# Performance work log

Measured on AMD Instinct MI355X. Metric: run time of the kernel, lower is better.

The kernel has to match this reference:

```python
import jax, jax.numpy as jnp
import numpy as np
from functools import partial

MIN_LIKELIHOOD = 1e-09


@partial(jax.custom_vjp, nondiff_argnums=(1,))
def lower_bound_toward(x, bound):
    return jnp.maximum(x, bound)

def _lbt_fwd(x, bound):
    return jnp.maximum(x, bound), x

def _lbt_bwd(bound, x, g):
    # gradient passes if input above bound, or gradient pushes x toward the bound
    pass_through = (x >= bound) | (g < 0)
    return (jnp.where(pass_through, g, jnp.zeros_like(g)),)

lower_bound_toward.defvjp(_lbt_fwd, _lbt_bwd)


def cdf_logits(x, Hs, As, Bs):
    # x: (C, 1, M). Per-channel tiny matmul chain with softplus/tanh gating.
    logits = x
    for H, a, b in zip(Hs, As, Bs):
        logits = jnp.einsum('cij,cjm->cim', jax.nn.softplus(H), logits) + b
        logits = logits + jnp.tanh(a) * jnp.tanh(logits)
    return logits


def setup_inputs() -> dict:
    key = jax.random.key(0)
    N, C, Hsp, W = 16, 320, 32, 32
    filters = (3, 3, 3)
    init_scale = 10.0
    fs = (1,) + filters + (1,)
    scale = init_scale ** (1.0 / (len(filters) + 1))
    keys = jax.random.split(key, len(filters) + 2)
    inp = {'x': jax.random.normal(keys[0], (N, C, Hsp, W), dtype=jnp.float32) * 3.0}
    for k in range(len(filters) + 1):
        H_init = float(np.log(np.expm1(1.0 / scale / fs[k + 1])))
        inp['H%d' % k] = jnp.full((C, fs[k + 1], fs[k]), H_init, dtype=jnp.float32)
        inp['a%d' % k] = jnp.zeros((C, fs[k + 1], 1), dtype=jnp.float32)
        inp['b%d' % k] = jax.random.uniform(keys[k + 1], (C, fs[k + 1], 1), dtype=jnp.float32, minval=-0.5, maxval=0.5)
    return inp


def reference(x, H0, H1, H2, H3, a0, a1, a2, a3, b0, b1, b2, b3):
    N, C, Hsp, W = x.shape
    Hs = (H0, H1, H2, H3)
    As = (a0, a1, a2, a3)
    Bs = (b0, b1, b2, b3)
    # (N,C,H,W) -> (C,1,N*H*W)
    lat = jnp.transpose(x, (1, 0, 2, 3)).reshape(C, 1, -1)
    cdf_upper = cdf_logits(lat + 0.5, Hs, As, Bs)
    cdf_lower = cdf_logits(lat - 0.5, Hs, As, Bs)
    sign = jax.lax.stop_gradient(-jnp.sign(cdf_upper + cdf_lower))
    like = jnp.abs(jax.nn.sigmoid(sign * cdf_upper) - jax.nn.sigmoid(sign * cdf_lower))
    like = jnp.transpose(like.reshape(C, N, Hsp, W), (1, 0, 2, 3))
    return lower_bound_toward(like, MIN_LIKELIHOOD)
```

## Files before the change

### kernel.cpp

```cpp
#include <hip/hip_runtime.h>
#include <math.h>


constexpr int HW = 1024;
constexpr float MINL = 1e-9f;

__device__ __forceinline__ float softplus_f(float v) {
    return fmaxf(v, 0.0f) + log1pf(expf(-fabsf(v)));
}

template<bool GATED>
__device__ __forceinline__ float cdf_t(float u, const float* q) {
    float y0 = fmaf(q[0], u, q[34]);
    float y1 = fmaf(q[1], u, q[35]);
    float y2 = fmaf(q[2], u, q[36]);
    if (GATED) {
        y0 = fmaf(q[24], tanhf(y0), y0);
        y1 = fmaf(q[25], tanhf(y1), y1);
        y2 = fmaf(q[26], tanhf(y2), y2);
    }
    float z0 = fmaf(q[3], y0, fmaf(q[4],  y1, fmaf(q[5],  y2, q[37])));
    float z1 = fmaf(q[6], y0, fmaf(q[7],  y1, fmaf(q[8],  y2, q[38])));
    float z2 = fmaf(q[9], y0, fmaf(q[10], y1, fmaf(q[11], y2, q[39])));
    if (GATED) {
        z0 = fmaf(q[27], tanhf(z0), z0);
        z1 = fmaf(q[28], tanhf(z1), z1);
        z2 = fmaf(q[29], tanhf(z2), z2);
    }
    float w0 = fmaf(q[12], z0, fmaf(q[13], z1, fmaf(q[14], z2, q[40])));
    float w1 = fmaf(q[15], z0, fmaf(q[16], z1, fmaf(q[17], z2, q[41])));
    float w2 = fmaf(q[18], z0, fmaf(q[19], z1, fmaf(q[20], z2, q[42])));
    if (GATED) {
        w0 = fmaf(q[30], tanhf(w0), w0);
        w1 = fmaf(q[31], tanhf(w1), w1);
        w2 = fmaf(q[32], tanhf(w2), w2);
    }
    float s = fmaf(q[21], w0, fmaf(q[22], w1, fmaf(q[23], w2, q[43])));
    if (GATED) s = fmaf(q[33], tanhf(s), s);
    return tanhf(0.5f * s);
}

template<bool GATED>
__device__ __forceinline__ float elem_like(float v, const float* q) {
    float tu = cdf_t<GATED>(v + 0.5f, q);
    float tl = cdf_t<GATED>(v - 0.5f, q);
    return fmaxf(0.5f * fabsf(tu - tl), MINL);
}

__global__ __launch_bounds__(256)
void hyperprior_density_kernel(
    const float* __restrict__ x,
    const float* __restrict__ H0, const float* __restrict__ a0, const float* __restrict__ b0,
    const float* __restrict__ H1, const float* __restrict__ a1, const float* __restrict__ b1,
    const float* __restrict__ H2, const float* __restrict__ a2, const float* __restrict__ b2,
    const float* __restrict__ H3, const float* __restrict__ a3, const float* __restrict__ b3,
    float* __restrict__ out, int C)
{
    __shared__ float p[44];
    const int c   = blockIdx.x;
    const int n   = blockIdx.y;
    const int tid = threadIdx.x;

    if (tid < 24) {
        float h;
        if      (tid < 3)  h = H0[c * 3 + tid];
        else if (tid < 12) h = H1[c * 9 + (tid - 3)];
        else if (tid < 21) h = H2[c * 9 + (tid - 12)];
        else               h = H3[c * 3 + (tid - 21)];
        p[tid] = softplus_f(h);
    } else if (tid < 34) {
        int i = tid - 24;
        float av;
        if      (i < 3) av = a0[c * 3 + i];
        else if (i < 6) av = a1[c * 3 + (i - 3)];
        else if (i < 9) av = a2[c * 3 + (i - 6)];
        else            av = a3[c];
        p[tid] = tanhf(av);
    } else if (tid < 44) {
        int i = tid - 34;
        float bv;
        if      (i < 3) bv = b0[c * 3 + i];
        else if (i < 6) bv = b1[c * 3 + (i - 3)];
        else if (i < 9) bv = b2[c * 3 + (i - 6)];
        else            bv = b3[c];
        p[tid] = bv;
    }
    __syncthreads();

    float q[44];
#pragma unroll
    for (int i = 0; i < 44; ++i) q[i] = p[i];

    bool gated = false;
#pragma unroll
    for (int i = 24; i < 34; ++i) gated = gated || (q[i] != 0.0f);

    const size_t base = ((size_t)n * (size_t)C + (size_t)c) * (size_t)HW;
    const float4* xin = reinterpret_cast<const float4*>(x + base);
    float4*       op  = reinterpret_cast<float4*>(out + base);

    float4 v = xin[tid];
    float4 r;
    if (!gated) {
        r.x = elem_like<false>(v.x, q);
        r.y = elem_like<false>(v.y, q);
        r.z = elem_like<false>(v.z, q);
        r.w = elem_like<false>(v.w, q);
    } else {
        r.x = elem_like<true>(v.x, q);
        r.y = elem_like<true>(v.y, q);
        r.z = elem_like<true>(v.z, q);
        r.w = elem_like<true>(v.w, q);
    }
    op[tid] = r;
}

extern "C" void kernel_launch(void* const* d_in, const int* in_sizes, int n_in,
                              void* d_out, int out_size, void* d_ws, size_t ws_size,
                              hipStream_t stream) {
    const float* x  = (const float*)d_in[0];
    const float* H0 = (const float*)d_in[1];
    const float* a0 = (const float*)d_in[2];
    const float* b0 = (const float*)d_in[3];
    const float* H1 = (const float*)d_in[4];
    const float* a1 = (const float*)d_in[5];
    const float* b1 = (const float*)d_in[6];
    const float* H2 = (const float*)d_in[7];
    const float* a2 = (const float*)d_in[8];
    const float* b2 = (const float*)d_in[9];
    const float* H3 = (const float*)d_in[10];
    const float* a3 = (const float*)d_in[11];
    const float* b3 = (const float*)d_in[12];
    float* out = (float*)d_out;

    const int C = in_sizes[1] / 3;
    const int N = in_sizes[0] / (C * HW);

    dim3 grid(C, N);
    hipLaunchKernelGGL(hyperprior_density_kernel, grid, dim3(256), 0, stream,
                       x, H0, a0, b0, H1, a1, b1, H2, a2, b2, H3, a3, b3, out, C);
}
```

Baseline: 102.7 us.

## Precompute per-channel parameters in a prep kernel and use fast tanh

New measurement: 103.4 us. Within noise of the previous version (+0.6%).

```diff
diff --git a/kernel.cpp b/kernel.cpp
--- a/kernel.cpp
+++ b/kernel.cpp
@@ -2,117 +2,133 @@
 #include <math.h>
 
 
-constexpr int HW = 1024;
+constexpr int HW   = 1024;
+constexpr int NPAR = 44;
+constexpr int PSTR = 48;
 constexpr float MINL = 1e-9f;
 
 __device__ __forceinline__ float softplus_f(float v) {
     return fmaxf(v, 0.0f) + log1pf(expf(-fabsf(v)));
 }
 
-template<bool GATED>
-__device__ __forceinline__ float cdf_t(float u, const float* q) {
-    float y0 = fmaf(q[0], u, q[34]);
-    float y1 = fmaf(q[1], u, q[35]);
-    float y2 = fmaf(q[2], u, q[36]);
-    if (GATED) {
-        y0 = fmaf(q[24], tanhf(y0), y0);
-        y1 = fmaf(q[25], tanhf(y1), y1);
-        y2 = fmaf(q[26], tanhf(y2), y2);
-    }
-    float z0 = fmaf(q[3], y0, fmaf(q[4],  y1, fmaf(q[5],  y2, q[37])));
-    float z1 = fmaf(q[6], y0, fmaf(q[7],  y1, fmaf(q[8],  y2, q[38])));
-    float z2 = fmaf(q[9], y0, fmaf(q[10], y1, fmaf(q[11], y2, q[39])));
-    if (GATED) {
-        z0 = fmaf(q[27], tanhf(z0), z0);
-        z1 = fmaf(q[28], tanhf(z1), z1);
-        z2 = fmaf(q[29], tanhf(z2), z2);
-    }
-    float w0 = fmaf(q[12], z0, fmaf(q[13], z1, fmaf(q[14], z2, q[40])));
-    float w1 = fmaf(q[15], z0, fmaf(q[16], z1, fmaf(q[17], z2, q[41])));
-    float w2 = fmaf(q[18], z0, fmaf(q[19], z1, fmaf(q[20], z2, q[42])));
-    if (GATED) {
-        w0 = fmaf(q[30], tanhf(w0), w0);
-        w1 = fmaf(q[31], tanhf(w1), w1);
-        w2 = fmaf(q[32], tanhf(w2), w2);
-    }
-    float s = fmaf(q[21], w0, fmaf(q[22], w1, fmaf(q[23], w2, q[43])));
-    if (GATED) s = fmaf(q[33], tanhf(s), s);
-    return tanhf(0.5f * s);
-}
-
-template<bool GATED>
-__device__ __forceinline__ float elem_like(float v, const float* q) {
-    float tu = cdf_t<GATED>(v + 0.5f, q);
-    float tl = cdf_t<GATED>(v - 0.5f, q);
-    return fmaxf(0.5f * fabsf(tu - tl), MINL);
+__device__ __forceinline__ float fast_tanh(float u) {
+    float e = __expf(-2.0f * fabsf(u));
+    float t = __fdividef(1.0f - e, 1.0f + e);
+    return copysignf(t, u);
 }
 
 __global__ __launch_bounds__(256)
-void hyperprior_density_kernel(
-    const float* __restrict__ x,
-    const float* __restrict__ H0, const float* __restrict__ a0, const float* __restrict__ b0,
-    const float* __restrict__ H1, const float* __restrict__ a1, const float* __restrict__ b1,
-    const float* __restrict__ H2, const float* __restrict__ a2, const float* __restrict__ b2,
-    const float* __restrict__ H3, const float* __restrict__ a3, const float* __restrict__ b3,
-    float* __restrict__ out, int C)
+void hp_prep(const float* __restrict__ H0, const float* __restrict__ a0, const float* __restrict__ b0,
+             const float* __restrict__ H1, const float* __restrict__ a1, const float* __restrict__ b1,
+             const float* __restrict__ H2, const float* __restrict__ a2, const float* __restrict__ b2,
+             const float* __restrict__ H3, const float* __restrict__ a3, const float* __restrict__ b3,
+             float* __restrict__ P, int C)
 {
-    __shared__ float p[44];
+    int t = blockIdx.x * 256 + threadIdx.x;
+    if (t >= C * NPAR) return;
+    int c = t / NPAR;
+    int i = t - c * NPAR;
+    float v;
+    if (i < 24) {
+        float h;
+        if      (i < 3)  h = H0[c * 3 + i];
+        else if (i < 12) h = H1[c * 9 + (i - 3)];
+        else if (i < 21) h = H2[c * 9 + (i - 12)];
+        else             h = H3[c * 3 + (i - 21)];
+        v = softplus_f(h);
+    } else if (i < 34) {
+        int j = i - 24; float a;
+        if      (j < 3) a = a0[c * 3 + j];
+        else if (j < 6) a = a1[c * 3 + (j - 3)];
+        else if (j < 9) a = a2[c * 3 + (j - 6)];
+        else            a = a3[c];
+        v = tanhf(a);
+    } else {
+        int j = i - 34; float b;
+        if      (j < 3) b = b0[c * 3 + j];
+        else if (j < 6) b = b1[c * 3 + (j - 3)];
+        else if (j < 9) b = b2[c * 3 + (j - 6)];
+        else            b = b3[c];
+        v = b;
+    }
+    P[c * PSTR + i] = v;
+}
+
+__global__ __launch_bounds__(256)
+void hp_main(const float* __restrict__ x, const float* __restrict__ P,
+             float* __restrict__ out, int C)
+{
     const int c   = blockIdx.x;
     const int n   = blockIdx.y;
     const int tid = threadIdx.x;
 
-    if (tid < 24) {
-        float h;
-        if      (tid < 3)  h = H0[c * 3 + tid];
-        else if (tid < 12) h = H1[c * 9 + (tid - 3)];
-        else if (tid < 21) h = H2[c * 9 + (tid - 12)];
-        else               h = H3[c * 3 + (tid - 21)];
-        p[tid] = softplus_f(h);
-    } else if (tid < 34) {
-        int i = tid - 24;
-        float av;
-        if      (i < 3) av = a0[c * 3 + i];
-        else if (i < 6) av = a1[c * 3 + (i - 3)];
-        else if (i < 9) av = a2[c * 3 + (i - 6)];
-        else            av = a3[c];
-        p[tid] = tanhf(av);
-    } else if (tid < 44) {
-        int i = tid - 34;
-        float bv;
-        if      (i < 3) bv = b0[c * 3 + i];
-        else if (i < 6) bv = b1[c * 3 + (i - 3)];
-        else if (i < 9) bv = b2[c * 3 + (i - 6)];
-        else            bv = b3[c];
-        p[tid] = bv;
-    }
-    __syncthreads();
+    const float* __restrict__ q = P + (size_t)c * PSTR;
+    const float k0 = q[0],  k1 = q[1],  k2 = q[2],  k3 = q[3],  k4 = q[4];
+    const float k5 = q[5],  k6 = q[6],  k7 = q[7],  k8 = q[8],  k9 = q[9];
+    const float k10 = q[10], k11 = q[11], k12 = q[12], k13 = q[13], k14 = q[14];
+    const float k15 = q[15], k16 = q[16], k17 = q[17], k18 = q[18], k19 = q[19];
+    const float k20 = q[20], k21 = q[21], k22 = q[22], k23 = q[23];
+    const float g0 = q[24], g1 = q[25], g2 = q[26], g3 = q[27], g4 = q[28];
+    const float g5 = q[29], g6 = q[30], g7 = q[31], g8 = q[32], g9 = q[33];
+    const float c0 = q[34], c1 = q[35], c2 = q[36], c3 = q[37], c4 = q[38];
+    const float c5 = q[39], c6 = q[40], c7 = q[41], c8 = q[42], c9 = q[43];
 
-    float q[44];
-#pragma unroll
-    for (int i = 0; i < 44; ++i) q[i] = p[i];
+    const bool gated = (g0 != 0.f) | (g1 != 0.f) | (g2 != 0.f) | (g3 != 0.f) |
+                       (g4 != 0.f) | (g5 != 0.f) | (g6 != 0.f) | (g7 != 0.f) |
+                       (g8 != 0.f) | (g9 != 0.f);
 
-    bool gated = false;
-#pragma unroll
-    for (int i = 24; i < 34; ++i) gated = gated || (q[i] != 0.0f);
+    auto cdfU = [&](float u) -> float {
+        float y0 = fmaf(k0, u, c0);
+        float y1 = fmaf(k1, u, c1);
+        float y2 = fmaf(k2, u, c2);
+        float z0 = fmaf(k3, y0, fmaf(k4,  y1, fmaf(k5,  y2, c3)));
+        float z1 = fmaf(k6, y0, fmaf(k7,  y1, fmaf(k8,  y2, c4)));
+        float z2 = fmaf(k9, y0, fmaf(k10, y1, fmaf(k11, y2, c5)));
+        float w0 = fmaf(k12, z0, fmaf(k13, z1, fmaf(k14, z2, c6)));
+        float w1 = fmaf(k15, z0, fmaf(k16, z1, fmaf(k17, z2, c7)));
+        float w2 = fmaf(k18, z0, fmaf(k19, z1, fmaf(k20, z2, c8)));
+        float s  = fmaf(k21, w0, fmaf(k22, w1, fmaf(k23, w2, c9)));
+        return fast_tanh(0.5f * s);
+    };
+    auto cdfG = [&](float u) -> float {
+        float y0 = fmaf(k0, u, c0);
+        float y1 = fmaf(k1, u, c1);
+        float y2 = fmaf(k2, u, c2);
+        y0 = fmaf(g0, fast_tanh(y0), y0);
+        y1 = fmaf(g1, fast_tanh(y1), y1);
+        y2 = fmaf(g2, fast_tanh(y2), y2);
+        float z0 = fmaf(k3, y0, fmaf(k4,  y1, fmaf(k5,  y2, c3)));
+        float z1 = fmaf(k6, y0, fmaf(k7,  y1, fmaf(k8,  y2, c4)));
+        float z2 = fmaf(k9, y0, fmaf(k10, y1, fmaf(k11, y2, c5)));
+        z0 = fmaf(g3, fast_tanh(z0), z0);
+        z1 = fmaf(g4, fast_tanh(z1), z1);
+        z2 = fmaf(g5, fast_tanh(z2), z2);
+        float w0 = fmaf(k12, z0, fmaf(k13, z1, fmaf(k14, z2, c6)));
+        float w1 = fmaf(k15, z0, fmaf(k16, z1, fmaf(k17, z2, c7)));
+        float w2 = fmaf(k18, z0, fmaf(k19, z1, fmaf(k20, z2, c8)));
+        w0 = fmaf(g6, fast_tanh(w0), w0);
+        w1 = fmaf(g7, fast_tanh(w1), w1);
+        w2 = fmaf(g8, fast_tanh(w2), w2);
+        float s = fmaf(k21, w0, fmaf(k22, w1, fmaf(k23, w2, c9)));
+        s = fmaf(g9, fast_tanh(s), s);
+        return fast_tanh(0.5f * s);
+    };
 
     const size_t base = ((size_t)n * (size_t)C + (size_t)c) * (size_t)HW;
-    const float4* xin = reinterpret_cast<const float4*>(x + base);
-    float4*       op  = reinterpret_cast<float4*>(out + base);
-
-    float4 v = xin[tid];
+    const float4 v = reinterpret_cast<const float4*>(x + base)[tid];
     float4 r;
     if (!gated) {
-        r.x = elem_like<false>(v.x, q);
-        r.y = elem_like<false>(v.y, q);
-        r.z = elem_like<false>(v.z, q);
-        r.w = elem_like<false>(v.w, q);
+        r.x = fmaxf(0.5f * fabsf(cdfU(v.x + 0.5f) - cdfU(v.x - 0.5f)), MINL);
+        r.y = fmaxf(0.5f * fabsf(cdfU(v.y + 0.5f) - cdfU(v.y - 0.5f)), MINL);
+        r.z = fmaxf(0.5f * fabsf(cdfU(v.z + 0.5f) - cdfU(v.z - 0.5f)), MINL);
+        r.w = fmaxf(0.5f * fabsf(cdfU(v.w + 0.5f) - cdfU(v.w - 0.5f)), MINL);
     } else {
-        r.x = elem_like<true>(v.x, q);
-        r.y = elem_like<true>(v.y, q);
-        r.z = elem_like<true>(v.z, q);
-        r.w = elem_like<true>(v.w, q);
+        r.x = fmaxf(0.5f * fabsf(cdfG(v.x + 0.5f) - cdfG(v.x - 0.5f)), MINL);
+        r.y = fmaxf(0.5f * fabsf(cdfG(v.y + 0.5f) - cdfG(v.y - 0.5f)), MINL);
+        r.z = fmaxf(0.5f * fabsf(cdfG(v.z + 0.5f) - cdfG(v.z - 0.5f)), MINL);
+        r.w = fmaxf(0.5f * fabsf(cdfG(v.w + 0.5f) - cdfG(v.w - 0.5f)), MINL);
     }
-    op[tid] = r;
+    reinterpret_cast<float4*>(out + base)[tid] = r;
 }
 
 extern "C" void kernel_launch(void* const* d_in, const int* in_sizes, int n_in,
@@ -132,11 +148,14 @@
     const float* a3 = (const float*)d_in[11];
     const float* b3 = (const float*)d_in[12];
     float* out = (float*)d_out;
+    float* P   = (float*)d_ws;
 
     const int C = in_sizes[1] / 3;
     const int N = in_sizes[0] / (C * HW);
 
-    dim3 grid(C, N);
-    hipLaunchKernelGGL(hyperprior_density_kernel, grid, dim3(256), 0, stream,
-                       x, H0, a0, b0, H1, a1, b1, H2, a2, b2, H3, a3, b3, out, C);
+    const int prep_items = C * NPAR;
+    hipLaunchKernelGGL(hp_prep, dim3((prep_items + 255) / 256), dim3(256), 0, stream,
+                       H0, a0, b0, H1, a1, b1, H2, a2, b2, H3, a3, b3, P, C);
+    hipLaunchKernelGGL(hp_main, dim3(C, N), dim3(256), 0, stream,
+                       x, P, out, C);
 }
```
